# Kernel tuning notes

Hardware: AMD Instinct MI355X
Metric: run time of the kernel (lower is better)

## Reference

```python
import jax, jax.numpy as jnp
import numpy as np

DIM = 1024
HEADS = 16
DIM_HEAD = 64
INNER = HEADS * DIM_HEAD
LN_EPS = 1e-5


def setup_inputs() -> dict:
    key = jax.random.key(0)
    ks = jax.random.split(key, 7)
    b, n = 2, 2048
    x = jax.random.normal(ks[0], (b, n, DIM), dtype=jnp.float32)
    attn_bias = jax.random.normal(ks[1], (HEADS, n, n), dtype=jnp.float32)
    gamma = jnp.ones((DIM,), dtype=jnp.float32)
    beta = jnp.zeros((DIM,), dtype=jnp.float32)
    wq = jax.random.normal(ks[2], (DIM, INNER), dtype=jnp.float32) * (DIM ** -0.5)
    wkv = jax.random.normal(ks[3], (DIM, 2 * INNER), dtype=jnp.float32) * (DIM ** -0.5)
    wo = jax.random.normal(ks[4], (INNER, DIM), dtype=jnp.float32) * (INNER ** -0.5)
    return {"x": x, "attn_bias": attn_bias, "gamma": gamma, "beta": beta,
            "wq": wq, "wkv": wkv, "wo": wo}


def reference(x, attn_bias, gamma, beta, wq, wkv, wo):
    b, n, _ = x.shape
    scale = DIM_HEAD ** -0.5
    # LayerNorm
    mu = jnp.mean(x, axis=-1, keepdims=True)
    var = jnp.var(x, axis=-1, keepdims=True)
    xn = (x - mu) * jax.lax.rsqrt(var + LN_EPS) * gamma + beta
    # QKV projections
    q = xn @ wq                      # [b, n, inner]
    kv = xn @ wkv                    # [b, n, 2*inner]
    k, v = jnp.split(kv, 2, axis=-1)
    split_heads = lambda t: t.reshape(b, n, HEADS, DIM_HEAD).transpose(0, 2, 1, 3)
    q, k, v = map(split_heads, (q, k, v))  # [b, h, n, d]
    q = q * scale
    sim = jnp.einsum('bhid,bhjd->bhij', q, k)
    sim = sim + attn_bias[None]      # broadcast over batch
    causal_mask = jnp.triu(jnp.ones((n, n), dtype=bool), k=1)
    sim = jnp.where(causal_mask, -jnp.finfo(sim.dtype).max, sim)
    attn = jax.nn.softmax(sim, axis=-1)
    out = jnp.einsum('bhij,bhjd->bhid', attn, v)
    out = out.transpose(0, 2, 1, 3).reshape(b, n, INNER)
    return out @ wo
```

## Files before the change

kernel.cpp:

```cpp
#include <hip/hip_runtime.h>
#include <hip/hip_bf16.h>

#define DIM   1024
#define HEADS 16
#define DHEAD 64
#define INNER 1024
#define NSEQ  2048
#define NB    2
#define MROWS (NB * NSEQ)
#define QS    (3 * INNER)

typedef __attribute__((ext_vector_type(8))) short    short8;
typedef __attribute__((ext_vector_type(4))) short    short4v;
typedef __attribute__((ext_vector_type(4))) float    floatx4;
typedef __attribute__((ext_vector_type(8))) _Float16 half8;

#define GLOBAL_AS __attribute__((address_space(1)))
#define LDS_AS    __attribute__((address_space(3)))

static __device__ __forceinline__ short f2h(float f) {
  _Float16 h = (_Float16)f;
  return __builtin_bit_cast(short, h);
}
static __device__ __forceinline__ float h2f(short s) {
  return (float)__builtin_bit_cast(_Float16, s);
}

static __device__ __forceinline__ floatx4 mfma16(short8 a, short8 b, floatx4 c) {
  return __builtin_amdgcn_mfma_f32_16x16x32_f16(
      __builtin_bit_cast(half8, a), __builtin_bit_cast(half8, b), c, 0, 0, 0);
}

__device__ __constant__ signed char kQtTab[40] = {
  15,14,13,12,11,10,9,8,7,6,5,4,3,
  15,14,13,12,11,10,9,8,7,
  15,14,13,12,11,
  15,
  2,6,10,14,
  1,5,9,13,
  0,4,8,12};
__device__ __constant__ signed char kCTab[40] = {
  0,0,0,0,0,0,0,0,0,0,0,0,0,
  1,1,1,1,1,1,1,1,1,
  2,2,2,2,2,
  3,
  0,1,2,3,
  0,1,2,3,
  0,1,2,3};
__device__ __constant__ signed char kSlotTab[16][4] = {
  {36,-1,-1,-1},{32,-1,-1,-1},{28,-1,-1,-1},{12,-1,-1,-1},
  {11,37,-1,-1},{10,33,-1,-1},{ 9,29,-1,-1},{ 8,21,-1,-1},
  { 7,20,38,-1},{ 6,19,34,-1},{ 5,18,30,-1},{ 4,17,26,-1},
  { 3,16,25,39},{ 2,15,24,35},{ 1,14,23,31},{ 0,13,22,27}};

__global__ __launch_bounds__(256) void ln_kernel(const float* __restrict__ x,
                                                 const float* __restrict__ gamma,
                                                 const float* __restrict__ beta,
                                                 short* __restrict__ xn) {
  int row = blockIdx.x;
  int t   = threadIdx.x;
  const float4* xr = reinterpret_cast<const float4*>(x + (size_t)row * DIM);
  float4 v = xr[t];
  float s  = v.x + v.y + v.z + v.w;
  float s2 = v.x * v.x + v.y * v.y + v.z * v.z + v.w * v.w;
#pragma unroll
  for (int off = 1; off < 64; off <<= 1) {
    s  += __shfl_xor(s, off);
    s2 += __shfl_xor(s2, off);
  }
  __shared__ float red[8];
  if ((t & 63) == 0) { red[t >> 6] = s; red[(t >> 6) + 4] = s2; }
  __syncthreads();
  s  = red[0] + red[1] + red[2] + red[3];
  s2 = red[4] + red[5] + red[6] + red[7];
  float mu   = s * (1.0f / DIM);
  float var  = s2 * (1.0f / DIM) - mu * mu;
  float rstd = rsqrtf(var + 1e-5f);
  float4 g  = reinterpret_cast<const float4*>(gamma)[t];
  float4 bb = reinterpret_cast<const float4*>(beta)[t];
  short4v o;
  o.x = f2h((v.x - mu) * rstd * g.x + bb.x);
  o.y = f2h((v.y - mu) * rstd * g.y + bb.y);
  o.z = f2h((v.z - mu) * rstd * g.z + bb.z);
  o.w = f2h((v.w - mu) * rstd * g.w + bb.w);
  reinterpret_cast<short4v*>(xn + (size_t)row * DIM)[t] = o;
}

__global__ __launch_bounds__(256) void transpose_f16(const float* __restrict__ w,
                                                     short* __restrict__ wt,
                                                     int Kk, int Nn) {
  __shared__ float tile[32][33];
  int n0 = blockIdx.x * 32, k0 = blockIdx.y * 32;
  int tx = threadIdx.x & 31, ty = threadIdx.x >> 5;
#pragma unroll
  for (int i = 0; i < 32; i += 8)
    tile[ty + i][tx] = w[(size_t)(k0 + ty + i) * Nn + n0 + tx];
  __syncthreads();
#pragma unroll
  for (int i = 0; i < 32; i += 8)
    wt[(size_t)(n0 + ty + i) * Kk + k0 + tx] = f2h(tile[tx][ty + i]);
}

template <bool F32OUT>
__global__ __launch_bounds__(256) void gemm_bt(const short* __restrict__ A,
                                               const short* __restrict__ Bt,
                                               void* __restrict__ Cout,
                                               int Nn, int Kk,
                                               float oscale, float oscale2,
                                               int qsplit) {
  constexpr int BM = 128, BN = 128, BK = 64;
  __shared__ __attribute__((aligned(16))) short As[BM * BK];
  __shared__ __attribute__((aligned(16))) short Bs[BN * BK];
  int bm = blockIdx.x, bn = blockIdx.y;
  int t = threadIdx.x, lane = t & 63, w = t >> 6;
  int l15 = lane & 15, lhi = lane >> 4;
  int wr = w >> 1, wc = w & 1;
  float osc = (bn * BN < qsplit) ? oscale : oscale2;
  floatx4 acc[4][4] = {};
  const short* Ag = A + (size_t)bm * BM * Kk;
  const short* Bg = Bt + (size_t)bn * BN * Kk;

  for (int k0 = 0; k0 < Kk; k0 += BK) {
#pragma unroll
    for (int it = 0; it < 4; ++it) {
      int base = it * 256 + w * 64;
      int idx  = base + lane;
      int row  = idx >> 3, kc = (idx & 7) << 3;
      __builtin_amdgcn_global_load_lds(
          (const GLOBAL_AS unsigned int*)(Ag + (size_t)row * Kk + k0 + kc),
          (LDS_AS unsigned int*)(As + base * 8), 16, 0, 0);
    }
#pragma unroll
    for (int it = 0; it < 4; ++it) {
      int base = it * 256 + w * 64;
      int idx  = base + lane;
      int row  = idx >> 3, kc = (idx & 7) << 3;
      __builtin_amdgcn_global_load_lds(
          (const GLOBAL_AS unsigned int*)(Bg + (size_t)row * Kk + k0 + kc),
          (LDS_AS unsigned int*)(Bs + base * 8), 16, 0, 0);
    }
    __syncthreads();
#pragma unroll
    for (int kc = 0; kc < 2; ++kc) {
      short8 a[4], b[4];
#pragma unroll
      for (int mt = 0; mt < 4; ++mt)
        a[mt] = *reinterpret_cast<const short8*>(
            &As[(wr * 64 + mt * 16 + l15) * BK + lhi * 8 + kc * 32]);
#pragma unroll
      for (int nt = 0; nt < 4; ++nt)
        b[nt] = *reinterpret_cast<const short8*>(
            &Bs[(wc * 64 + nt * 16 + l15) * BK + lhi * 8 + kc * 32]);
#pragma unroll
      for (int mt = 0; mt < 4; ++mt)
#pragma unroll
        for (int nt = 0; nt < 4; ++nt)
          acc[mt][nt] = mfma16(a[mt], b[nt], acc[mt][nt]);
    }
    __syncthreads();
  }

  int row0 = bm * BM + wr * 64;
  int col0 = bn * BN + wc * 64;
#pragma unroll
  for (int mt = 0; mt < 4; ++mt)
#pragma unroll
    for (int nt = 0; nt < 4; ++nt)
#pragma unroll
      for (int r = 0; r < 4; ++r) {
        int row = row0 + mt * 16 + lhi * 4 + r;
        int col = col0 + nt * 16 + l15;
        if (F32OUT)
          ((float*)Cout)[(size_t)row * Nn + col] = acc[mt][nt][r] * osc;
        else
          ((short*)Cout)[(size_t)row * Nn + col] = f2h(acc[mt][nt][r] * osc);
      }
}

__global__ __launch_bounds__(512) void attn_kernel(const short* __restrict__ qkv,
                                                   const float* __restrict__ bias,
                                                   short* __restrict__ Opart,
                                                   float* __restrict__ mlpart) {
  constexpr int LDK = 72;
  __shared__ __attribute__((aligned(16))) short Ks[2][64 * LDK];
  __shared__ __attribute__((aligned(16))) short Vt[2][64 * LDK];
  __shared__ __attribute__((aligned(16))) short Ps[128 * LDK];

  int g = blockIdx.x;
  int gg = g >> 4, slot = g & 15;
  int b = slot >> 3;
  int p = gg * 8 + (slot & 7);
  int h = p / 40, id = p % 40;
  int qt = kQtTab[id], c = kCTab[id];
  int tt0 = c * 8;
  int tt1 = 2 * qt + 2; if (tt0 + 8 < tt1) tt1 = tt0 + 8;
  int qb = qt * 128;

  int t = threadIdx.x, lane = t & 63, w = t >> 6;
  int l15 = lane & 15, lhi = lane >> 4;

  const short* qrow =
      qkv + ((size_t)(b * NSEQ + qb + w * 16 + l15)) * QS + h * DHEAD + lhi * 8;
  short8 qf0 = *reinterpret_cast<const short8*>(qrow);
  short8 qf1 = *reinterpret_cast<const short8*>(qrow + 32);

  int krow = t >> 3, kcol = (t & 7) << 3;
  int vrr = (t >> 4) * 2, vcc = (t & 15) << 2;
  short8 kr;
  short4v vr0, vr1;

  auto issue_kv = [&](int tile) {
    int j0 = tile * 64;
    kr = *reinterpret_cast<const short8*>(
        qkv + ((size_t)(b * NSEQ + j0 + krow)) * QS + INNER + h * DHEAD + kcol);
    const short* vp = qkv + ((size_t)(b * NSEQ + j0 + vrr)) * QS +
                      2 * INNER + h * DHEAD + vcc;
    vr0 = *reinterpret_cast<const short4v*>(vp);
    vr1 = *reinterpret_cast<const short4v*>(vp + QS);
  };
  auto issue_bias = [&](int tile, floatx4 (&br)[4]) {
    const float* bb =
        bias + ((size_t)h * NSEQ + (qb + w * 16 + l15)) * NSEQ + tile * 64 + lhi * 4;
#pragma unroll
    for (int jt = 0; jt < 4; ++jt)
      br[jt] = *reinterpret_cast<const floatx4*>(bb + jt * 16);
  };
  auto writeKV = [&](int buf) {
    *reinterpret_cast<short8*>(&Ks[buf][krow * LDK + kcol]) = kr;
#pragma unroll
    for (int e = 0; e < 4; ++e) {
      int d  = vcc + e;
      int jj = vrr ^ (((d >> 3) & 7) << 3);
      unsigned int pk = (unsigned short)vr0[e] |
                        ((unsigned int)(unsigned short)vr1[e] << 16);
      *reinterpret_cast<unsigned int*>(&Vt[buf][d * LDK + jj]) = pk;
    }
  };

  float m = -1e30f, l = 0.f;
  floatx4 oacc[4] = {};

  auto step = [&](int tt, int buf, floatx4 (&br)[4]) {
    if (tt + 1 < tt1) issue_kv(tt + 1);
    __syncthreads();

    floatx4 s[4];
#pragma unroll
    for (int jt = 0; jt < 4; ++jt) s[jt] = br[jt];
    if (tt + 2 < tt1) issue_bias(tt + 2, br);

#pragma unroll
    for (int jt = 0; jt < 4; ++jt) {
      short8 kf0 = *reinterpret_cast<const short8*>(
          &Ks[buf][(jt * 16 + l15) * LDK + lhi * 8]);
      short8 kf1 = *reinterpret_cast<const short8*>(
          &Ks[buf][(jt * 16 + l15) * LDK + lhi * 8 + 32]);
      s[jt] = mfma16(kf0, qf0, s[jt]);
      s[jt] = mfma16(kf1, qf1, s[jt]);
    }

    if (tt >= 2 * qt) {
      int dq = qb + w * 16 + l15 - tt * 64;
#pragma unroll
      for (int jt = 0; jt < 4; ++jt)
#pragma unroll
        for (int r = 0; r < 4; ++r) {
          int jloc = jt * 16 + lhi * 4 + r;
          if (jloc > dq) s[jt][r] = -1e30f;
        }
    }

    float mx = s[0][0];
#pragma unroll
    for (int jt = 0; jt < 4; ++jt)
#pragma unroll
      for (int r = 0; r < 4; ++r) mx = fmaxf(mx, s[jt][r]);
    mx = fmaxf(mx, __shfl_xor(mx, 16));
    mx = fmaxf(mx, __shfl_xor(mx, 32));
    float mnew = fmaxf(m, mx);
    float fac  = __expf(m - mnew);
    m = mnew;
    float ps = 0.f;
#pragma unroll
    for (int jt = 0; jt < 4; ++jt)
#pragma unroll
      for (int r = 0; r < 4; ++r) {
        float pv = __expf(s[jt][r] - mnew);
        s[jt][r] = pv;
        ps += pv;
      }
    ps += __shfl_xor(ps, 16);
    ps += __shfl_xor(ps, 32);
    l = l * fac + ps;

    float facr[4];
#pragma unroll
    for (int r = 0; r < 4; ++r)
      facr[r] = __shfl(fac, (lane & 48) | (lhi * 4 + r));
#pragma unroll
    for (int dt = 0; dt < 4; ++dt)
#pragma unroll
      for (int r = 0; r < 4; ++r) oacc[dt][r] *= facr[r];

#pragma unroll
    for (int jt = 0; jt < 4; ++jt) {
      short4v pv4;
      pv4.x = f2h(s[jt][0]); pv4.y = f2h(s[jt][1]);
      pv4.z = f2h(s[jt][2]); pv4.w = f2h(s[jt][3]);
      *reinterpret_cast<short4v*>(
          &Ps[(w * 16 + l15) * LDK + jt * 16 + lhi * 4]) = pv4;
    }

#pragma unroll
    for (int jc = 0; jc < 2; ++jc) {
      short8 pf = *reinterpret_cast<const short8*>(
          &Ps[(w * 16 + l15) * LDK + lhi * 8 + jc * 32]);
#pragma unroll
      for (int dt = 0; dt < 4; ++dt) {
        int dd = dt * 16 + l15;
        int jj = (lhi * 8 + jc * 32) ^ (((dd >> 3) & 7) << 3);
        short8 vf = *reinterpret_cast<const short8*>(&Vt[buf][dd * LDK + jj]);
        oacc[dt] = mfma16(pf, vf, oacc[dt]);
      }
    }

    if (tt + 1 < tt1) writeKV(buf ^ 1);
  };

  floatx4 brA[4], brB[4];
  issue_kv(tt0);
  issue_bias(tt0, brA);
  issue_bias(tt0 + 1, brB);
  writeKV(0);

  int nt = tt1 - tt0;
  for (int i = 0; i < nt; i += 2) {
    step(tt0 + i, 0, brA);
    step(tt0 + i + 1, 1, brB);
  }

  size_t pp = (size_t)(b * HEADS + h) * 40 + id;
  short* Ob = Opart + pp * 8192;
#pragma unroll
  for (int dt = 0; dt < 4; ++dt)
#pragma unroll
    for (int r = 0; r < 4; ++r)
      Ob[(w * 16 + lhi * 4 + r) * 64 + dt * 16 + l15] = f2h(oacc[dt][r]);
  if (lhi == 0) {
    mlpart[pp * 256 + w * 16 + l15] = m;
    mlpart[pp * 256 + 128 + w * 16 + l15] = l;
  }
}

__global__ __launch_bounds__(512) void attn_combine(const short* __restrict__ Opart,
                                                    const float* __restrict__ mlpart,
                                                    short* __restrict__ o) {
  int qt = blockIdx.x, h = blockIdx.y, b = blockIdx.z;
  int nc = qt / 4 + 1;
  int t = threadIdx.x, row = t >> 2, cg = (t & 3) << 4;
  size_t base = (size_t)(b * HEADS + h) * 40;

  float mv[4], lv[4];
  float M = -1e30f;
#pragma unroll
  for (int c2 = 0; c2 < 4; ++c2) {
    if (c2 < nc) {
      size_t p = base + kSlotTab[qt][c2];
      mv[c2] = mlpart[p * 256 + row];
      lv[c2] = mlpart[p * 256 + 128 + row];
      M = fmaxf(M, mv[c2]);
    }
  }

  float acc[16] = {};
  float lsum = 0.f;
#pragma unroll
  for (int c2 = 0; c2 < 4; ++c2) {
    if (c2 >= nc) break;
    float wgt = __expf(mv[c2] - M);
    lsum += wgt * lv[c2];
    size_t p = base + kSlotTab[qt][c2];
    const short8* Or =
        reinterpret_cast<const short8*>(Opart + p * 8192 + row * 64 + cg);
    short8 a0 = Or[0], a1 = Or[1];
#pragma unroll
    for (int e = 0; e < 8; ++e) {
      acc[e]     += wgt * h2f(a0[e]);
      acc[8 + e] += wgt * h2f(a1[e]);
    }
  }
  float inv = 1.f / lsum;
  short* op = o + ((size_t)(b * NSEQ + qt * 128 + row)) * INNER + h * DHEAD + cg;
  short8 o0, o1;
#pragma unroll
  for (int e = 0; e < 8; ++e) {
    o0[e] = f2h(acc[e] * inv);
    o1[e] = f2h(acc[8 + e] * inv);
  }
  reinterpret_cast<short8*>(op)[0] = o0;
  reinterpret_cast<short8*>(op)[1] = o1;
}

extern "C" void kernel_launch(void* const* d_in, const int* in_sizes, int n_in,
                              void* d_out, int out_size, void* d_ws, size_t ws_size,
                              hipStream_t stream) {
  const float* x     = (const float*)d_in[0];
  const float* bias  = (const float*)d_in[1];
  const float* gamma = (const float*)d_in[2];
  const float* beta  = (const float*)d_in[3];
  const float* wq    = (const float*)d_in[4];
  const float* wkv   = (const float*)d_in[5];
  const float* wo    = (const float*)d_in[6];
  float* out = (float*)d_out;

  char* ws = (char*)d_ws;
  const size_t MB = 1024 * 1024;
  short* xn      = (short*)(ws);
  short* wqkv_t  = (short*)(ws + 8  * MB);
  short* wo_t    = (short*)(ws + 14 * MB);
  short* qkv     = (short*)(ws + 16 * MB);
  short* Opart   = (short*)(ws + 40 * MB);
  float* mlpart  = (float*)(ws + 62 * MB);
  short* ao      = xn;

  ln_kernel<<<MROWS, 256, 0, stream>>>(x, gamma, beta, xn);
  transpose_f16<<<dim3(INNER / 32, DIM / 32), 256, 0, stream>>>(wq, wqkv_t, DIM, INNER);
  transpose_f16<<<dim3(2 * INNER / 32, DIM / 32), 256, 0, stream>>>(
      wkv, wqkv_t + (size_t)1024 * 1024, DIM, 2 * INNER);
  transpose_f16<<<dim3(DIM / 32, INNER / 32), 256, 0, stream>>>(wo, wo_t, INNER, DIM);

  gemm_bt<false><<<dim3(MROWS / 128, QS / 128), 256, 0, stream>>>(
      xn, wqkv_t, qkv, QS, DIM, 0.125f, 1.0f, 1024);

  attn_kernel<<<1280, 512, 0, stream>>>(qkv, bias, Opart, mlpart);
  attn_combine<<<dim3(16, HEADS, NB), 512, 0, stream>>>(Opart, mlpart, ao);

  gemm_bt<true><<<dim3(MROWS / 128, DIM / 128), 256, 0, stream>>>(
      ao, wo_t, out, DIM, INNER, 1.0f, 1.0f, 0);
}
```

Measured before the change: 180.3 us.

## Process both batches per attention block to share bias loads; write direct outputs

Each attention block now handles both batch elements for one head and query chunk. The attn_bias tile, which is shared across the batch, is loaded once and used twice, halving bias traffic and the grid size. K tiles are now moved into XOR-swizzled LDS with direct global-to-LDS loads. Chunks that cover the whole causal range now normalise and write straight to the output, so the combine kernel only runs for the later query tiles. The cost is more registers and two extra barriers per step, since V now has a single buffer, and the block count drops from 1280 to 640.

```diff
diff --git a/kernel.cpp b/kernel.cpp
--- a/kernel.cpp
+++ b/kernel.cpp
@@ -179,195 +179,240 @@
 
 __global__ __launch_bounds__(512) void attn_kernel(const short* __restrict__ qkv,
                                                    const float* __restrict__ bias,
+                                                   short* __restrict__ ao,
                                                    short* __restrict__ Opart,
                                                    float* __restrict__ mlpart) {
-  constexpr int LDK = 72;
-  __shared__ __attribute__((aligned(16))) short Ks[2][64 * LDK];
-  __shared__ __attribute__((aligned(16))) short Vt[2][64 * LDK];
-  __shared__ __attribute__((aligned(16))) short Ps[128 * LDK];
-
-  int g = blockIdx.x;
-  int gg = g >> 4, slot = g & 15;
-  int b = slot >> 3;
-  int p = gg * 8 + (slot & 7);
-  int h = p / 40, id = p % 40;
-  int qt = kQtTab[id], c = kCTab[id];
+  __shared__ __attribute__((aligned(16))) short Ks[2][2][4096];
+  __shared__ __attribute__((aligned(16))) short Vt[2][4096];
+  __shared__ __attribute__((aligned(16))) short Ps[128 * 72];
+
+  int p = blockIdx.x;
+  int rank = p >> 4, h = p & 15;
+  int qt = kQtTab[rank], c = kCTab[rank];
   int tt0 = c * 8;
   int tt1 = 2 * qt + 2; if (tt0 + 8 < tt1) tt1 = tt0 + 8;
   int qb = qt * 128;
-
   int t = threadIdx.x, lane = t & 63, w = t >> 6;
   int l15 = lane & 15, lhi = lane >> 4;
 
-  const short* qrow =
-      qkv + ((size_t)(b * NSEQ + qb + w * 16 + l15)) * QS + h * DHEAD + lhi * 8;
-  short8 qf0 = *reinterpret_cast<const short8*>(qrow);
-  short8 qf1 = *reinterpret_cast<const short8*>(qrow + 32);
-
-  int krow = t >> 3, kcol = (t & 7) << 3;
+  short8 qf[2][2];
+#pragma unroll
+  for (int bb = 0; bb < 2; ++bb) {
+    const short* qrow = qkv +
+        ((size_t)(bb * NSEQ + qb + w * 16 + l15)) * QS + h * DHEAD + lhi * 8;
+    qf[bb][0] = *reinterpret_cast<const short8*>(qrow);
+    qf[bb][1] = *reinterpret_cast<const short8*>(qrow + 32);
+  }
+
+  int krow = t >> 3;
+  int kcg  = (t & 7) ^ (krow & 7);
   int vrr = (t >> 4) * 2, vcc = (t & 15) << 2;
-  short8 kr;
-  short4v vr0, vr1;
-
-  auto issue_kv = [&](int tile) {
-    int j0 = tile * 64;
-    kr = *reinterpret_cast<const short8*>(
-        qkv + ((size_t)(b * NSEQ + j0 + krow)) * QS + INNER + h * DHEAD + kcol);
-    const short* vp = qkv + ((size_t)(b * NSEQ + j0 + vrr)) * QS +
-                      2 * INNER + h * DHEAD + vcc;
-    vr0 = *reinterpret_cast<const short4v*>(vp);
-    vr1 = *reinterpret_cast<const short4v*>(vp + QS);
+  short4v vr[2][2];
+
+  auto issueK = [&](int tile, int nb) {
+#pragma unroll
+    for (int bb = 0; bb < 2; ++bb) {
+      const short* gp = qkv +
+          ((size_t)(bb * NSEQ + tile * 64 + krow)) * QS + INNER + h * DHEAD + kcg * 8;
+      __builtin_amdgcn_global_load_lds(
+          (const GLOBAL_AS unsigned int*)gp,
+          (LDS_AS unsigned int*)(&Ks[nb][bb][0] + (size_t)w * 512), 16, 0, 0);
+    }
   };
-  auto issue_bias = [&](int tile, floatx4 (&br)[4]) {
-    const float* bb =
-        bias + ((size_t)h * NSEQ + (qb + w * 16 + l15)) * NSEQ + tile * 64 + lhi * 4;
+  auto issueV = [&](int tile) {
+#pragma unroll
+    for (int bb = 0; bb < 2; ++bb) {
+      const short* vp = qkv + ((size_t)(bb * NSEQ + tile * 64 + vrr)) * QS +
+                        2 * INNER + h * DHEAD + vcc;
+      vr[bb][0] = *reinterpret_cast<const short4v*>(vp);
+      vr[bb][1] = *reinterpret_cast<const short4v*>(vp + QS);
+    }
+  };
+  auto writeV = [&]() {
+#pragma unroll
+    for (int bb = 0; bb < 2; ++bb)
+#pragma unroll
+      for (int e = 0; e < 4; ++e) {
+        int d  = vcc + e;
+        int jj = vrr ^ ((d & 7) << 3);
+        unsigned int pk = (unsigned short)vr[bb][0][e] |
+                          ((unsigned int)(unsigned short)vr[bb][1][e] << 16);
+        *reinterpret_cast<unsigned int*>(&Vt[bb][d * 64 + jj]) = pk;
+      }
+  };
+  auto issueB = [&](int tile, floatx4 (&br)[4]) {
+    const float* bb0 = bias +
+        ((size_t)h * NSEQ + (qb + w * 16 + l15)) * NSEQ + tile * 64 + lhi * 4;
 #pragma unroll
     for (int jt = 0; jt < 4; ++jt)
-      br[jt] = *reinterpret_cast<const floatx4*>(bb + jt * 16);
+      br[jt] = *reinterpret_cast<const floatx4*>(bb0 + jt * 16);
   };
-  auto writeKV = [&](int buf) {
-    *reinterpret_cast<short8*>(&Ks[buf][krow * LDK + kcol]) = kr;
-#pragma unroll
-    for (int e = 0; e < 4; ++e) {
-      int d  = vcc + e;
-      int jj = vrr ^ (((d >> 3) & 7) << 3);
-      unsigned int pk = (unsigned short)vr0[e] |
-                        ((unsigned int)(unsigned short)vr1[e] << 16);
-      *reinterpret_cast<unsigned int*>(&Vt[buf][d * LDK + jj]) = pk;
+
+  float m[2], l[2];
+  floatx4 oacc[2][4] = {};
+#pragma unroll
+  for (int bb = 0; bb < 2; ++bb) { m[bb] = -1e30f; l[bb] = 0.f; }
+
+  int swz = (l15 & 7) << 3;
+
+  auto step = [&](int tt, int KB, floatx4 (&brU)[4], floatx4 (&brN)[4]) {
+    bool more = (tt + 1 < tt1);
+    if (more) { issueK(tt + 1, KB ^ 1); issueV(tt + 1); issueB(tt + 1, brN); }
+
+#pragma unroll
+    for (int bb = 0; bb < 2; ++bb) {
+      floatx4 s[4];
+#pragma unroll
+      for (int jt = 0; jt < 4; ++jt) s[jt] = brU[jt];
+
+#pragma unroll
+      for (int jt = 0; jt < 4; ++jt) {
+        int ro = (jt * 16 + l15) * 64;
+        short8 k0 = *reinterpret_cast<const short8*>(
+            &Ks[KB][bb][ro + ((lhi * 8) ^ swz)]);
+        short8 k1 = *reinterpret_cast<const short8*>(
+            &Ks[KB][bb][ro + ((lhi * 8 + 32) ^ swz)]);
+        s[jt] = mfma16(k0, qf[bb][0], s[jt]);
+        s[jt] = mfma16(k1, qf[bb][1], s[jt]);
+      }
+
+      if (tt >= 2 * qt) {
+        int dq = qb + w * 16 + l15 - tt * 64;
+#pragma unroll
+        for (int jt = 0; jt < 4; ++jt)
+#pragma unroll
+          for (int r = 0; r < 4; ++r)
+            if (jt * 16 + lhi * 4 + r > dq) s[jt][r] = -1e30f;
+      }
+
+      float mx = s[0][0];
+#pragma unroll
+      for (int jt = 0; jt < 4; ++jt)
+#pragma unroll
+        for (int r = 0; r < 4; ++r) mx = fmaxf(mx, s[jt][r]);
+      mx = fmaxf(mx, __shfl_xor(mx, 16));
+      mx = fmaxf(mx, __shfl_xor(mx, 32));
+      float mnew = fmaxf(m[bb], mx);
+      float fac  = __expf(m[bb] - mnew);
+      m[bb] = mnew;
+      float ps = 0.f;
+#pragma unroll
+      for (int jt = 0; jt < 4; ++jt)
+#pragma unroll
+        for (int r = 0; r < 4; ++r) {
+          float pv = __expf(s[jt][r] - mnew);
+          s[jt][r] = pv;
+          ps += pv;
+        }
+      ps += __shfl_xor(ps, 16);
+      ps += __shfl_xor(ps, 32);
+      l[bb] = l[bb] * fac + ps;
+
+      float facr[4];
+#pragma unroll
+      for (int r = 0; r < 4; ++r)
+        facr[r] = __shfl(fac, (lane & 48) | (lhi * 4 + r));
+#pragma unroll
+      for (int dt = 0; dt < 4; ++dt)
+#pragma unroll
+        for (int r = 0; r < 4; ++r) oacc[bb][dt][r] *= facr[r];
+
+#pragma unroll
+      for (int jt = 0; jt < 4; ++jt) {
+        short4v pv4;
+        pv4.x = f2h(s[jt][0]); pv4.y = f2h(s[jt][1]);
+        pv4.z = f2h(s[jt][2]); pv4.w = f2h(s[jt][3]);
+        *reinterpret_cast<short4v*>(
+            &Ps[(w * 16 + l15) * 72 + jt * 16 + lhi * 4]) = pv4;
+      }
+
+#pragma unroll
+      for (int jc = 0; jc < 2; ++jc) {
+        short8 pf = *reinterpret_cast<const short8*>(
+            &Ps[(w * 16 + l15) * 72 + lhi * 8 + jc * 32]);
+#pragma unroll
+        for (int dt = 0; dt < 4; ++dt) {
+          int dd = dt * 16 + l15;
+          short8 vf = *reinterpret_cast<const short8*>(
+              &Vt[bb][dd * 64 + ((lhi * 8 + jc * 32) ^ swz)]);
+          oacc[bb][dt] = mfma16(pf, vf, oacc[bb][dt]);
+        }
+      }
+    }
+
+    if (more) {
+      __syncthreads();
+      writeV();
+      __syncthreads();
     }
   };
 
-  float m = -1e30f, l = 0.f;
-  floatx4 oacc[4] = {};
-
-  auto step = [&](int tt, int buf, floatx4 (&br)[4]) {
-    if (tt + 1 < tt1) issue_kv(tt + 1);
-    __syncthreads();
-
-    floatx4 s[4];
-#pragma unroll
-    for (int jt = 0; jt < 4; ++jt) s[jt] = br[jt];
-    if (tt + 2 < tt1) issue_bias(tt + 2, br);
-
-#pragma unroll
-    for (int jt = 0; jt < 4; ++jt) {
-      short8 kf0 = *reinterpret_cast<const short8*>(
-          &Ks[buf][(jt * 16 + l15) * LDK + lhi * 8]);
-      short8 kf1 = *reinterpret_cast<const short8*>(
-          &Ks[buf][(jt * 16 + l15) * LDK + lhi * 8 + 32]);
-      s[jt] = mfma16(kf0, qf0, s[jt]);
-      s[jt] = mfma16(kf1, qf1, s[jt]);
-    }
-
-    if (tt >= 2 * qt) {
-      int dq = qb + w * 16 + l15 - tt * 64;
-#pragma unroll
-      for (int jt = 0; jt < 4; ++jt)
-#pragma unroll
-        for (int r = 0; r < 4; ++r) {
-          int jloc = jt * 16 + lhi * 4 + r;
-          if (jloc > dq) s[jt][r] = -1e30f;
-        }
-    }
-
-    float mx = s[0][0];
-#pragma unroll
-    for (int jt = 0; jt < 4; ++jt)
-#pragma unroll
-      for (int r = 0; r < 4; ++r) mx = fmaxf(mx, s[jt][r]);
-    mx = fmaxf(mx, __shfl_xor(mx, 16));
-    mx = fmaxf(mx, __shfl_xor(mx, 32));
-    float mnew = fmaxf(m, mx);
-    float fac  = __expf(m - mnew);
-    m = mnew;
-    float ps = 0.f;
-#pragma unroll
-    for (int jt = 0; jt < 4; ++jt)
-#pragma unroll
-      for (int r = 0; r < 4; ++r) {
-        float pv = __expf(s[jt][r] - mnew);
-        s[jt][r] = pv;
-        ps += pv;
-      }
-    ps += __shfl_xor(ps, 16);
-    ps += __shfl_xor(ps, 32);
-    l = l * fac + ps;
-
-    float facr[4];
-#pragma unroll
-    for (int r = 0; r < 4; ++r)
-      facr[r] = __shfl(fac, (lane & 48) | (lhi * 4 + r));
-#pragma unroll
-    for (int dt = 0; dt < 4; ++dt)
-#pragma unroll
-      for (int r = 0; r < 4; ++r) oacc[dt][r] *= facr[r];
-
-#pragma unroll
-    for (int jt = 0; jt < 4; ++jt) {
-      short4v pv4;
-      pv4.x = f2h(s[jt][0]); pv4.y = f2h(s[jt][1]);
-      pv4.z = f2h(s[jt][2]); pv4.w = f2h(s[jt][3]);
-      *reinterpret_cast<short4v*>(
-          &Ps[(w * 16 + l15) * LDK + jt * 16 + lhi * 4]) = pv4;
-    }
-
-#pragma unroll
-    for (int jc = 0; jc < 2; ++jc) {
-      short8 pf = *reinterpret_cast<const short8*>(
-          &Ps[(w * 16 + l15) * LDK + lhi * 8 + jc * 32]);
-#pragma unroll
-      for (int dt = 0; dt < 4; ++dt) {
-        int dd = dt * 16 + l15;
-        int jj = (lhi * 8 + jc * 32) ^ (((dd >> 3) & 7) << 3);
-        short8 vf = *reinterpret_cast<const short8*>(&Vt[buf][dd * LDK + jj]);
-        oacc[dt] = mfma16(pf, vf, oacc[dt]);
-      }
-    }
-
-    if (tt + 1 < tt1) writeKV(buf ^ 1);
-  };
-
   floatx4 brA[4], brB[4];
-  issue_kv(tt0);
-  issue_bias(tt0, brA);
-  issue_bias(tt0 + 1, brB);
-  writeKV(0);
+  issueK(tt0, 0);
+  issueV(tt0);
+  issueB(tt0, brA);
+  __syncthreads();
+  writeV();
+  __syncthreads();
 
   int nt = tt1 - tt0;
   for (int i = 0; i < nt; i += 2) {
-    step(tt0 + i, 0, brA);
-    step(tt0 + i + 1, 1, brB);
-  }
-
-  size_t pp = (size_t)(b * HEADS + h) * 40 + id;
-  short* Ob = Opart + pp * 8192;
-#pragma unroll
-  for (int dt = 0; dt < 4; ++dt)
-#pragma unroll
-    for (int r = 0; r < 4; ++r)
-      Ob[(w * 16 + lhi * 4 + r) * 64 + dt * 16 + l15] = f2h(oacc[dt][r]);
-  if (lhi == 0) {
-    mlpart[pp * 256 + w * 16 + l15] = m;
-    mlpart[pp * 256 + 128 + w * 16 + l15] = l;
+    step(tt0 + i, 0, brA, brB);
+    step(tt0 + i + 1, 1, brB, brA);
+  }
+
+  bool single = (tt0 == 0) && (tt1 == 2 * qt + 2);
+  if (single) {
+#pragma unroll
+    for (int bb = 0; bb < 2; ++bb) {
+      float linv = 1.f / l[bb];
+      float lr[4];
+#pragma unroll
+      for (int r = 0; r < 4; ++r)
+        lr[r] = __shfl(linv, (lane & 48) | (lhi * 4 + r));
+#pragma unroll
+      for (int dt = 0; dt < 4; ++dt)
+#pragma unroll
+        for (int r = 0; r < 4; ++r) {
+          int row = qb + w * 16 + lhi * 4 + r;
+          int col = h * DHEAD + dt * 16 + l15;
+          ao[((size_t)(bb * NSEQ + row)) * INNER + col] =
+              f2h(oacc[bb][dt][r] * lr[r]);
+        }
+    }
+  } else {
+#pragma unroll
+    for (int bb = 0; bb < 2; ++bb) {
+      size_t pp = ((size_t)h * 40 + rank) * 2 + bb;
+      short* Ob = Opart + pp * 8192;
+#pragma unroll
+      for (int dt = 0; dt < 4; ++dt)
+#pragma unroll
+        for (int r = 0; r < 4; ++r)
+          Ob[(w * 16 + lhi * 4 + r) * 64 + dt * 16 + l15] = f2h(oacc[bb][dt][r]);
+      if (lhi == 0) {
+        mlpart[pp * 256 + w * 16 + l15] = m[bb];
+        mlpart[pp * 256 + 128 + w * 16 + l15] = l[bb];
+      }
+    }
   }
 }
 
 __global__ __launch_bounds__(512) void attn_combine(const short* __restrict__ Opart,
                                                     const float* __restrict__ mlpart,
                                                     short* __restrict__ o) {
-  int qt = blockIdx.x, h = blockIdx.y, b = blockIdx.z;
-  int nc = qt / 4 + 1;
+  int qt = blockIdx.x + 4, h = blockIdx.y, b = blockIdx.z;
+  int nc = (2 * qt + 9) >> 3;
   int t = threadIdx.x, row = t >> 2, cg = (t & 3) << 4;
-  size_t base = (size_t)(b * HEADS + h) * 40;
 
   float mv[4], lv[4];
   float M = -1e30f;
 #pragma unroll
   for (int c2 = 0; c2 < 4; ++c2) {
     if (c2 < nc) {
-      size_t p = base + kSlotTab[qt][c2];
-      mv[c2] = mlpart[p * 256 + row];
-      lv[c2] = mlpart[p * 256 + 128 + row];
+      size_t pp = ((size_t)h * 40 + kSlotTab[qt][c2]) * 2 + b;
+      mv[c2] = mlpart[pp * 256 + row];
+      lv[c2] = mlpart[pp * 256 + 128 + row];
       M = fmaxf(M, mv[c2]);
     }
   }
@@ -379,9 +424,9 @@
     if (c2 >= nc) break;
     float wgt = __expf(mv[c2] - M);
     lsum += wgt * lv[c2];
-    size_t p = base + kSlotTab[qt][c2];
+    size_t pp = ((size_t)h * 40 + kSlotTab[qt][c2]) * 2 + b;
     const short8* Or =
-        reinterpret_cast<const short8*>(Opart + p * 8192 + row * 64 + cg);
+        reinterpret_cast<const short8*>(Opart + pp * 8192 + row * 64 + cg);
     short8 a0 = Or[0], a1 = Or[1];
 #pragma unroll
     for (int e = 0; e < 8; ++e) {
@@ -432,8 +477,8 @@
   gemm_bt<false><<<dim3(MROWS / 128, QS / 128), 256, 0, stream>>>(
       xn, wqkv_t, qkv, QS, DIM, 0.125f, 1.0f, 1024);
 
-  attn_kernel<<<1280, 512, 0, stream>>>(qkv, bias, Opart, mlpart);
-  attn_combine<<<dim3(16, HEADS, NB), 512, 0, stream>>>(Opart, mlpart, ao);
+  attn_kernel<<<640, 512, 0, stream>>>(qkv, bias, ao, Opart, mlpart);
+  attn_combine<<<dim3(12, HEADS, NB), 512, 0, stream>>>(Opart, mlpart, ao);
 
   gemm_bt<true><<<dim3(MROWS / 128, DIM / 128), 256, 0, stream>>>(
       ao, wo_t, out, DIM, INNER, 1.0f, 1.0f, 0);
```

After: 172.5 us. 1.05x faster.
